# Performance work log

Measured on AMD Instinct MI355X. Metric: run time of the kernel, lower is better.

Reference implementation:

```python
import jax, jax.numpy as jnp
import numpy as np

K = 11          # k_size in the original module
HALF = K // 2   # 5
N_SIGNAL = 33554432  # 2**25 elements, 128 MB fp32


def setup_inputs() -> dict:
    key = jax.random.key(0)
    k1, _ = jax.random.split(key)
    x = jax.random.normal(k1, (N_SIGNAL,), dtype=jnp.float32)
    # learned parameter of Dilation1D(s=1.5)
    scale = jnp.asarray(1.5, dtype=jnp.float32)
    return {"x": x, "scale": scale}


def reference(x, scale):
    # parabolic structuring element: z = -5..5, h = -z^2 / (4*scale)
    z = jnp.linspace(-(K // 2), K // 2, K, dtype=jnp.float32)  # torch: -k//2+1 .. k//2 == -5..5
    h = -(z * z) / (4.0 * scale)  # [K]

    n = x.shape[0]
    pad = jnp.full((HALF,), -jnp.inf, dtype=x.dtype)
    xp = jnp.concatenate([pad, x, pad])  # [n + K - 1], -inf edge handling == original branches

    # out[r] = max_j ( x[r - HALF + j] + h[j] )  (max-plus / grayscale dilation)
    out = xp[0:n] + h[0]
    for j in range(1, K):  # fixed small K, unrolled window — no data-dim loop
        out = jnp.maximum(out, xp[j:j + n] + h[j])
    return out
```

## Files before the change

kernel.cpp:

```cpp
#include <hip/hip_runtime.h>
#include <math.h>


#define BLOCK   256
#define WPB     (BLOCK / 64)
#define QPT     4
#define TQ      60

__global__ __launch_bounds__(BLOCK) void dilate1d_kernel(
    const float4* __restrict__ x4,
    const float*  __restrict__ scale_p,
    float4*       __restrict__ out4,
    int n4,
    int ntiles)
{
    const int lane = threadIdx.x & 63;
    const int wid  = blockIdx.x * WPB + (threadIdx.x >> 6);
    const int tau0 = wid * QPT;
    if (tau0 >= ntiles) return;

    const float  NEG  = -INFINITY;
    const float4 NEG4 = make_float4(NEG, NEG, NEG, NEG);

    float4 v[QPT];
    const int gbase = tau0 * TQ - 2 + lane;
    const bool interior = (tau0 > 0) && (tau0 + QPT <= ntiles) &&
                          ((tau0 + QPT - 1) * TQ + 62 <= n4);
    if (interior) {
#pragma unroll
        for (int t = 0; t < QPT; ++t)
            v[t] = x4[gbase + t * TQ];
    } else {
#pragma unroll
        for (int t = 0; t < QPT; ++t) {
            int g = gbase + t * TQ;
            v[t] = ((tau0 + t) < ntiles && g >= 0 && g < n4) ? x4[g] : NEG4;
        }
    }

    const float r4s = 1.0f / (4.0f * scale_p[0]);
    const float hp1 = -1.0f  * r4s;
    const float hp2 = -4.0f  * r4s;
    const float hp3 = -9.0f  * r4s;
    const float hp4 = -16.0f * r4s;
    const float hp5 = -25.0f * r4s;

    const bool storelane = (lane >= 2) && (lane < 62);

#pragma unroll
    for (int t = 0; t < QPT; ++t) {
        const int tau = tau0 + t;
        if (tau >= ntiles) break;
        const float4 c = v[t];

        float w[14];
        w[0]  = __shfl_up(c.w, 2);
        w[1]  = __shfl_up(c.x, 1);
        w[2]  = __shfl_up(c.y, 1);
        w[3]  = __shfl_up(c.z, 1);
        w[4]  = __shfl_up(c.w, 1);
        w[5]  = c.x;  w[6] = c.y;  w[7] = c.z;  w[8] = c.w;
        w[9]  = __shfl_down(c.x, 1);
        w[10] = __shfl_down(c.y, 1);
        w[11] = __shfl_down(c.z, 1);
        w[12] = __shfl_down(c.w, 1);
        w[13] = __shfl_down(c.x, 2);

        float4 o;
        float* op = &o.x;
#pragma unroll
        for (int i = 0; i < 4; ++i) {
            const int cc = 5 + i;
            float m = w[cc];
            m = fmaxf(m, hp1 + fmaxf(w[cc - 1], w[cc + 1]));
            m = fmaxf(m, hp2 + fmaxf(w[cc - 2], w[cc + 2]));
            m = fmaxf(m, hp3 + fmaxf(w[cc - 3], w[cc + 3]));
            m = fmaxf(m, hp4 + fmaxf(w[cc - 4], w[cc + 4]));
            m = fmaxf(m, hp5 + fmaxf(w[cc - 5], w[cc + 5]));
            op[i] = m;
        }

        const int q = tau * TQ + (lane - 2);
        if (storelane && q < n4) out4[q] = o;
    }
}

extern "C" void kernel_launch(void* const* d_in, const int* in_sizes, int n_in,
                              void* d_out, int out_size, void* d_ws, size_t ws_size,
                              hipStream_t stream) {
    const float* x       = (const float*)d_in[0];
    const float* scale_p = (const float*)d_in[1];
    float*       out     = (float*)d_out;

    int n      = in_sizes[0];
    int n4     = n / 4;
    int ntiles = (n4 + TQ - 1) / TQ;
    int waves  = (ntiles + QPT - 1) / QPT;
    int blocks = (waves + WPB - 1) / WPB;

    dilate1d_kernel<<<blocks, BLOCK, 0, stream>>>(
        (const float4*)x, scale_p, (float4*)out, n4, ntiles);
}
```

Before: 230.3 us.

## Replace wave-shuffle halo exchange with overlapping float4 loads in grid-stride loop

Each thread now loads five consecutive float4 values directly, covering its own quad plus two neighbours on each side, instead of loading one quad and exchanging halos with cross-lane shuffles. This removes the 2 of every 64 lanes per wave that only supplied halo data and stored nothing. The launch also becomes a persistent grid-stride loop capped at 2048 blocks, with each thread handling two quads per tile. In exchange, every thread issues five times as many global load instructions, and the extra traffic relies on cache hits for the overlapping reads. The capped grid may also leave fewer waves in flight to hide memory latency.

```diff
diff --git a/kernel.cpp b/kernel.cpp
--- a/kernel.cpp
+++ b/kernel.cpp
@@ -3,9 +3,34 @@
 
 
 #define BLOCK   256
-#define WPB     (BLOCK / 64)
-#define QPT     4
-#define TQ      60
+#define QPT     2
+#define TILEQ   (BLOCK * QPT)
+#define MAXGRID 2048
+
+__device__ __forceinline__ float4 dilate_quad(
+    const float4* L,
+    float hp1, float hp2, float hp3, float hp4, float hp5)
+{
+    float w[20];
+#pragma unroll
+    for (int r = 0; r < 5; ++r) {
+        w[4*r+0] = L[r].x; w[4*r+1] = L[r].y;
+        w[4*r+2] = L[r].z; w[4*r+3] = L[r].w;
+    }
+    float4 o; float* op = &o.x;
+#pragma unroll
+    for (int i = 0; i < 4; ++i) {
+        const int c = 8 + i;
+        float m = w[c];
+        m = fmaxf(m, hp1 + fmaxf(w[c-1], w[c+1]));
+        m = fmaxf(m, hp2 + fmaxf(w[c-2], w[c+2]));
+        m = fmaxf(m, hp3 + fmaxf(w[c-3], w[c+3]));
+        m = fmaxf(m, hp4 + fmaxf(w[c-4], w[c+4]));
+        m = fmaxf(m, hp5 + fmaxf(w[c-5], w[c+5]));
+        op[i] = m;
+    }
+    return o;
+}
 
 __global__ __launch_bounds__(BLOCK) void dilate1d_kernel(
     const float4* __restrict__ x4,
@@ -14,29 +39,8 @@
     int n4,
     int ntiles)
 {
-    const int lane = threadIdx.x & 63;
-    const int wid  = blockIdx.x * WPB + (threadIdx.x >> 6);
-    const int tau0 = wid * QPT;
-    if (tau0 >= ntiles) return;
-
     const float  NEG  = -INFINITY;
     const float4 NEG4 = make_float4(NEG, NEG, NEG, NEG);
-
-    float4 v[QPT];
-    const int gbase = tau0 * TQ - 2 + lane;
-    const bool interior = (tau0 > 0) && (tau0 + QPT <= ntiles) &&
-                          ((tau0 + QPT - 1) * TQ + 62 <= n4);
-    if (interior) {
-#pragma unroll
-        for (int t = 0; t < QPT; ++t)
-            v[t] = x4[gbase + t * TQ];
-    } else {
-#pragma unroll
-        for (int t = 0; t < QPT; ++t) {
-            int g = gbase + t * TQ;
-            v[t] = ((tau0 + t) < ntiles && g >= 0 && g < n4) ? x4[g] : NEG4;
-        }
-    }
 
     const float r4s = 1.0f / (4.0f * scale_p[0]);
     const float hp1 = -1.0f  * r4s;
@@ -45,43 +49,35 @@
     const float hp4 = -16.0f * r4s;
     const float hp5 = -25.0f * r4s;
 
-    const bool storelane = (lane >= 2) && (lane < 62);
+    for (int tile = blockIdx.x; tile < ntiles; tile += gridDim.x) {
+        const int t0 = tile * TILEQ;
+        const int q0 = t0 + threadIdx.x;
+        const int q1 = q0 + BLOCK;
 
+        float4 A[5], B[5];
+        const bool interior = (t0 >= 2) && (t0 + TILEQ + 2 <= n4);
+        if (interior) {
+            const float4* pa = x4 + (q0 - 2);
+            const float4* pb = x4 + (q1 - 2);
 #pragma unroll
-    for (int t = 0; t < QPT; ++t) {
-        const int tau = tau0 + t;
-        if (tau >= ntiles) break;
-        const float4 c = v[t];
-
-        float w[14];
-        w[0]  = __shfl_up(c.w, 2);
-        w[1]  = __shfl_up(c.x, 1);
-        w[2]  = __shfl_up(c.y, 1);
-        w[3]  = __shfl_up(c.z, 1);
-        w[4]  = __shfl_up(c.w, 1);
-        w[5]  = c.x;  w[6] = c.y;  w[7] = c.z;  w[8] = c.w;
-        w[9]  = __shfl_down(c.x, 1);
-        w[10] = __shfl_down(c.y, 1);
-        w[11] = __shfl_down(c.z, 1);
-        w[12] = __shfl_down(c.w, 1);
-        w[13] = __shfl_down(c.x, 2);
-
-        float4 o;
-        float* op = &o.x;
+            for (int r = 0; r < 5; ++r) A[r] = pa[r];
 #pragma unroll
-        for (int i = 0; i < 4; ++i) {
-            const int cc = 5 + i;
-            float m = w[cc];
-            m = fmaxf(m, hp1 + fmaxf(w[cc - 1], w[cc + 1]));
-            m = fmaxf(m, hp2 + fmaxf(w[cc - 2], w[cc + 2]));
-            m = fmaxf(m, hp3 + fmaxf(w[cc - 3], w[cc + 3]));
-            m = fmaxf(m, hp4 + fmaxf(w[cc - 4], w[cc + 4]));
-            m = fmaxf(m, hp5 + fmaxf(w[cc - 5], w[cc + 5]));
-            op[i] = m;
+            for (int r = 0; r < 5; ++r) B[r] = pb[r];
+        } else {
+#pragma unroll
+            for (int r = 0; r < 5; ++r) {
+                int g = q0 - 2 + r;
+                A[r] = (g >= 0 && g < n4) ? x4[g] : NEG4;
+            }
+#pragma unroll
+            for (int r = 0; r < 5; ++r) {
+                int g = q1 - 2 + r;
+                B[r] = (g >= 0 && g < n4) ? x4[g] : NEG4;
+            }
         }
 
-        const int q = tau * TQ + (lane - 2);
-        if (storelane && q < n4) out4[q] = o;
+        out4[q0] = dilate_quad(A, hp1, hp2, hp3, hp4, hp5);
+        out4[q1] = dilate_quad(B, hp1, hp2, hp3, hp4, hp5);
     }
 }
 
@@ -94,10 +90,9 @@
 
     int n      = in_sizes[0];
     int n4     = n / 4;
-    int ntiles = (n4 + TQ - 1) / TQ;
-    int waves  = (ntiles + QPT - 1) / QPT;
-    int blocks = (waves + WPB - 1) / WPB;
+    int ntiles = (n4 + TILEQ - 1) / TILEQ;
+    int grid   = ntiles < MAXGRID ? ntiles : MAXGRID;
 
-    dilate1d_kernel<<<blocks, BLOCK, 0, stream>>>(
+    dilate1d_kernel<<<grid, BLOCK, 0, stream>>>(
         (const float4*)x, scale_p, (float4*)out, n4, ntiles);
 }
```

After: 233.4 us. Within noise of the previous version (+1.4%).
